# Kernel optimization log

Measured on AMD Instinct MI355X. Metric: run time of the kernel, lower is better.

Reference implementation:

```python
import jax, jax.numpy as jnp
import numpy as np

NEG_SLOPE = 0.2  # LeakyReLU slope used by GAT attention
EPS = 1e-16


def gat_conv(x, edge_index, W, a_src, a_dst, b):
    """One GATConv layer with 'mean' head aggregation.
    x: [N, Fin], edge_index: [2, E] (row 0 = src/j, row 1 = dst/i),
    W: [Fin, H*F], a_src/a_dst: [H, F], b: [F].
    Returns [N, F].
    """
    N = x.shape[0]
    H, F = a_src.shape
    h = (x @ W).reshape(N, H, F)                      # [N, H, F]
    src, dst = edge_index[0], edge_index[1]
    # per-node attention halves, gathered per edge
    as_ = jnp.einsum('nhf,hf->nh', h, a_src)          # [N, H]
    ad_ = jnp.einsum('nhf,hf->nh', h, a_dst)          # [N, H]
    e = jax.nn.leaky_relu(as_[src] + ad_[dst], NEG_SLOPE)  # [E, H]
    # segment softmax over incoming edges of each dst node
    m = jax.ops.segment_max(e, dst, num_segments=N)   # [N, H]
    ex = jnp.exp(e - m[dst])                          # [E, H]
    denom = jax.ops.segment_sum(ex, dst, num_segments=N)
    alpha = ex / (denom[dst] + EPS)                   # [E, H]
    # weighted scatter-aggregate of source features
    out = jax.ops.segment_sum(alpha[:, :, None] * h[src], dst, num_segments=N)  # [N, H, F]
    return out.mean(axis=1) + b                       # mean over heads


def setup_inputs() -> dict:
    key = jax.random.key(0)
    ks = jax.random.split(key, 10)
    N, E = 100000, 1000000
    in_dim, hid, out_dim, H = 128, 32, 16, 4
    x = jax.random.normal(ks[0], (N, in_dim), dtype=jnp.float32)
    edge_index = jax.random.randint(ks[1], (2, E), 0, N, dtype=jnp.int64)
    s1 = 1.0 / np.sqrt(in_dim)
    s2 = 1.0 / np.sqrt(hid)
    W1 = jax.random.uniform(ks[2], (in_dim, H * hid), jnp.float32, -s1, s1)
    a1_src = jax.random.uniform(ks[3], (H, hid), jnp.float32, -s2, s2)
    a1_dst = jax.random.uniform(ks[4], (H, hid), jnp.float32, -s2, s2)
    b1 = jnp.zeros((hid,), jnp.float32)
    s3 = 1.0 / np.sqrt(out_dim)
    W2 = jax.random.uniform(ks[5], (hid, H * out_dim), jnp.float32, -s2, s2)
    a2_src = jax.random.uniform(ks[6], (H, out_dim), jnp.float32, -s3, s3)
    a2_dst = jax.random.uniform(ks[7], (H, out_dim), jnp.float32, -s3, s3)
    b2 = jnp.zeros((out_dim,), jnp.float32)
    return {"x": x, "edge_index": edge_index,
            "W1": W1, "a1_src": a1_src, "a1_dst": a1_dst, "b1": b1,
            "W2": W2, "a2_src": a2_src, "a2_dst": a2_dst, "b2": b2}


def reference(x, edge_index, W1, a1_src, a1_dst, b1, W2, a2_src, a2_dst, b2):
    h = gat_conv(x, edge_index, W1, a1_src, a1_dst, b1)
    h = jax.nn.relu(h)
    # dropout is identity in eval mode
    out = gat_conv(h, edge_index, W2, a2_src, a2_dst, b2)
    return out
```

## Files before the change

### kernel.cpp

```cpp
#include <hip/hip_runtime.h>
#include <math.h>

#define NEG_SLOPE 0.2f
#define EPS_GAT 1e-16f
#define LOG2E 1.4426950408889634f
typedef unsigned int u32;
typedef unsigned short u16;
typedef __attribute__((ext_vector_type(8))) short short8;
typedef __attribute__((ext_vector_type(4))) float f32x4;

__device__ inline u16 f2bf(float x) {
    union { float f; u32 u; } v; v.f = x;
    u32 r = v.u + 0x7FFFu + ((v.u >> 16) & 1u);
    return (u16)(r >> 16);
}
__device__ inline float bf_lo(u32 u) {
    union { u32 i; float f; } v; v.i = u << 16; return v.f;
}
__device__ inline float bf_hi(u32 u) {
    union { u32 i; float f; } v; v.i = u & 0xFFFF0000u; return v.f;
}
__device__ inline float bf1(u16 s) {
    union { u32 i; float f; } v; v.i = ((u32)s) << 16; return v.f;
}
__device__ inline float fast_exp2(float x) {
#if __has_builtin(__builtin_amdgcn_exp2f)
    return __builtin_amdgcn_exp2f(x);
#else
    return exp2f(x);
#endif
}
__device__ inline float lrelu_exp2(float t) {
    return fast_exp2(fmaxf(t, NEG_SLOPE * t));
}


__global__ void degree_prep_kernel(const int* __restrict__ dst, int E,
                                   int* __restrict__ counts, int* __restrict__ rank,
                                   const float* __restrict__ W1,
                                   u16* __restrict__ w1t_hi, u16* __restrict__ w1t_lo,
                                   const float* __restrict__ W2, const float* __restrict__ a2s,
                                   const float* __restrict__ a2d, float* __restrict__ w_as,
                                   float* __restrict__ w_ad, int degBlocks) {
    int b = blockIdx.x;
    if (b < degBlocks) {
        int e = b * 256 + threadIdx.x;
        if (e < E) rank[e] = atomicAdd(&counts[dst[e]], 1);
    } else if (b < degBlocks + 64) {
        int i = (b - degBlocks) * 256 + threadIdx.x;
        int k = i >> 7, n = i & 127;
        float w = W1[i];
        u16 hi = f2bf(w);
        u16 lo = f2bf(w - bf1(hi));
        w1t_hi[n * 128 + k] = hi;
        w1t_lo[n * 128 + k] = lo;
    } else {
        int t = threadIdx.x;
        if (t < 128) {
            int h = t >> 5, k = t & 31;
            float s1 = 0.f, s2 = 0.f;
#pragma unroll
            for (int f = 0; f < 16; ++f) {
                float w = W2[k * 64 + h * 16 + f];
                s1 += w * a2s[h * 16 + f];
                s2 += w * a2d[h * 16 + f];
            }
            w_as[h * 32 + k] = s1;
            w_ad[h * 32 + k] = s2;
        }
    }
}

__global__ __launch_bounds__(1024) void scan_block_kernel(const int* __restrict__ counts, int N,
                                                          int* __restrict__ scanned, int* __restrict__ bsums) {
    __shared__ int tmp[1024];
    int i = blockIdx.x * 1024 + threadIdx.x;
    int v = (i < N) ? counts[i] : 0;
    tmp[threadIdx.x] = v;
    __syncthreads();
    for (int d = 1; d < 1024; d <<= 1) {
        int t = (threadIdx.x >= d) ? tmp[threadIdx.x - d] : 0;
        __syncthreads();
        tmp[threadIdx.x] += t;
        __syncthreads();
    }
    if (i < N) scanned[i] = tmp[threadIdx.x];
    if (threadIdx.x == 1023) bsums[blockIdx.x] = tmp[1023];
}

__global__ __launch_bounds__(256) void scan_partials_kernel(int* __restrict__ bsums, int nb) {
    __shared__ int tmp[256];
    int tid = threadIdx.x;
    int v = (tid < nb) ? bsums[tid] : 0;
    tmp[tid] = v;
    __syncthreads();
    for (int d = 1; d < 256; d <<= 1) {
        int t = (tid >= d) ? tmp[tid - d] : 0;
        __syncthreads();
        tmp[tid] += t;
        __syncthreads();
    }
    if (tid < nb) bsums[tid] = tmp[tid] - v;
}

__global__ void finalize_offsets_kernel(const int* __restrict__ scanned,
                                        const int* __restrict__ bsums_excl, int N,
                                        int* __restrict__ row_off) {
    int i = blockIdx.x * blockDim.x + threadIdx.x;
    if (i < N) {
        int incl = scanned[i] + bsums_excl[i >> 10];
        row_off[i + 1] = incl;
        if (i == 0) row_off[0] = 0;
    }
}

__global__ void fill_csr_kernel(const int* __restrict__ src, const int* __restrict__ dst, int E,
                                const int* __restrict__ row_off, const int* __restrict__ rank,
                                int* __restrict__ csr_src) {
    int e = blockIdx.x * blockDim.x + threadIdx.x;
    if (e < E) {
        int pos = row_off[dst[e]] + rank[e];
        csr_src[pos] = src[e];
    }
}


__global__ __launch_bounds__(256) void gemm1_mfma_kernel(const float* __restrict__ X,
                                                         const u16* __restrict__ w1t_hi,
                                                         const u16* __restrict__ w1t_lo,
                                                         const float* __restrict__ a_src,
                                                         const float* __restrict__ a_dst,
                                                         u16* __restrict__ Hb,
                                                         float* __restrict__ as_,
                                                         float* __restrict__ ad_, int N) {
    __shared__ u16 xsh_hi[64][40];
    __shared__ u16 xsh_lo[64][40];
    __shared__ u16 wbuf[10240];
    __shared__ float ash[128], adsh[128];
    u16* wsh_hi = wbuf;
    u16* wsh_lo = wbuf + 5120;
    int tid = threadIdx.x;
    int wave = tid >> 6, lane = tid & 63, quad = lane >> 4;
    int m0 = blockIdx.x * 64;

    if (tid < 128) { ash[tid] = a_src[tid]; adsh[tid] = a_dst[tid]; }

    f32x4 acc[4][2];
#pragma unroll
    for (int rt = 0; rt < 4; ++rt)
#pragma unroll
        for (int ct = 0; ct < 2; ++ct) acc[rt][ct] = (f32x4)(0.f);

    int xrow = tid >> 2, xkq = (tid & 3) * 8;

    for (int k0 = 0; k0 < 128; k0 += 32) {
        {
            int gr = m0 + xrow;
            float f[8];
            *(float4*)&f[0] = (gr < N) ? *(const float4*)(X + (size_t)gr * 128 + k0 + xkq)
                                       : make_float4(0.f, 0.f, 0.f, 0.f);
            *(float4*)&f[4] = (gr < N) ? *(const float4*)(X + (size_t)gr * 128 + k0 + xkq + 4)
                                       : make_float4(0.f, 0.f, 0.f, 0.f);
            u16 hi[8], lo[8];
#pragma unroll
            for (int i = 0; i < 8; ++i) {
                hi[i] = f2bf(f[i]);
                lo[i] = f2bf(f[i] - bf1(hi[i]));
            }
            *(uint4*)&xsh_hi[xrow][xkq] = *(uint4*)hi;
            *(uint4*)&xsh_lo[xrow][xkq] = *(uint4*)lo;
        }
        {
#pragma unroll
            for (int i = 0; i < 2; ++i) {
                int id = tid * 2 + i;
                int n = id >> 2, part = id & 3;
                *(uint4*)&wsh_hi[n * 40 + part * 8] =
                    ((const uint4*)(w1t_hi + n * 128 + k0))[part];
                *(uint4*)&wsh_lo[n * 40 + part * 8] =
                    ((const uint4*)(w1t_lo + n * 128 + k0))[part];
            }
        }
        __syncthreads();

        short8 bhi[2], blo[2];
#pragma unroll
        for (int ct = 0; ct < 2; ++ct) {
            int n = wave * 32 + ct * 16 + (lane & 15);
            bhi[ct] = *(const short8*)&wsh_hi[n * 40 + quad * 8];
            blo[ct] = *(const short8*)&wsh_lo[n * 40 + quad * 8];
        }
#pragma unroll
        for (int rt = 0; rt < 4; ++rt) {
            int m = rt * 16 + (lane & 15);
            short8 ahi = *(const short8*)&xsh_hi[m][quad * 8];
            short8 alo = *(const short8*)&xsh_lo[m][quad * 8];
#pragma unroll
            for (int ct = 0; ct < 2; ++ct) {
                acc[rt][ct] = __builtin_amdgcn_mfma_f32_16x16x32_bf16(ahi, bhi[ct], acc[rt][ct], 0, 0, 0);
                acc[rt][ct] = __builtin_amdgcn_mfma_f32_16x16x32_bf16(alo, bhi[ct], acc[rt][ct], 0, 0, 0);
                acc[rt][ct] = __builtin_amdgcn_mfma_f32_16x16x32_bf16(ahi, blo[ct], acc[rt][ct], 0, 0, 0);
            }
        }
        __syncthreads();
    }

    const int HS = 130;
#pragma unroll
    for (int rt = 0; rt < 4; ++rt)
#pragma unroll
        for (int ct = 0; ct < 2; ++ct) {
            int col = wave * 32 + ct * 16 + (lane & 15);
#pragma unroll
            for (int r = 0; r < 4; ++r) {
                int row = rt * 16 + quad * 4 + r;
                u16 hv = f2bf(acc[rt][ct][r]);
                int gr = m0 + row;
                if (gr < N) Hb[(size_t)gr * 128 + col] = hv;
                wbuf[row * HS + col] = hv;
            }
        }
    __syncthreads();

    {
        int row = tid >> 2, h = tid & 3;
        int gr = m0 + row;
        if (gr < N) {
            const u32* hr = (const u32*)&wbuf[row * HS + h * 32];
            float s1 = 0.f, s2 = 0.f;
#pragma unroll
            for (int q = 0; q < 16; ++q) {
                u32 u = hr[q];
                float flo = bf_lo(u), fhi = bf_hi(u);
                s1 += flo * ash[h * 32 + 2 * q] + fhi * ash[h * 32 + 2 * q + 1];
                s2 += flo * adsh[h * 32 + 2 * q] + fhi * adsh[h * 32 + 2 * q + 1];
            }
            as_[(size_t)gr * 4 + h] = s1 * LOG2E;
            ad_[(size_t)gr * 4 + h] = s2 * LOG2E;
        }
    }
}


__global__ __launch_bounds__(256) void node_agg128_kernel(const u32* __restrict__ Hb,
                                                          const float* __restrict__ as_,
                                                          const float* __restrict__ ad_,
                                                          const int* __restrict__ row_off,
                                                          const int* __restrict__ csr_src,
                                                          const float* __restrict__ bias,
                                                          const float* __restrict__ w_as,
                                                          const float* __restrict__ w_ad,
                                                          u32* __restrict__ O1,
                                                          float* __restrict__ as2,
                                                          float* __restrict__ ad2, int N) {
    int lane = threadIdx.x & 63;
    int node = __builtin_amdgcn_readfirstlane(blockIdx.x * 4 + (threadIdx.x >> 6));
    if (node >= N) return;
    int start = __builtin_amdgcn_readfirstlane(row_off[node]);
    int end   = __builtin_amdgcn_readfirstlane(row_off[node + 1]);
    int deg = end - start;
    int h = lane >> 4;
    float adh = ad_[node * 4 + h];

    int clamp = (deg > 0) ? deg - 1 : 0;
    int vidx = csr_src[start + min(lane, clamp)];
    int m = min(deg, 64);

    float2 acc = make_float2(0.f, 0.f);
    float den = 0.f;
    int j = 0;
    for (; j + 4 <= m; j += 4) {
        int s0 = __builtin_amdgcn_readlane(vidx, j);
        int s1 = __builtin_amdgcn_readlane(vidx, j + 1);
        int s2 = __builtin_amdgcn_readlane(vidx, j + 2);
        int s3 = __builtin_amdgcn_readlane(vidx, j + 3);
        float a0 = as_[s0 * 4 + h], a1 = as_[s1 * 4 + h];
        float a2 = as_[s2 * 4 + h], a3 = as_[s3 * 4 + h];
        u32 u0 = Hb[s0 * 64 + lane];
        u32 u1 = Hb[s1 * 64 + lane];
        u32 u2 = Hb[s2 * 64 + lane];
        u32 u3 = Hb[s3 * 64 + lane];
        float e0 = lrelu_exp2(a0 + adh), e1 = lrelu_exp2(a1 + adh);
        float e2 = lrelu_exp2(a2 + adh), e3 = lrelu_exp2(a3 + adh);
        acc.x = fmaf(e0, bf_lo(u0), acc.x); acc.y = fmaf(e0, bf_hi(u0), acc.y); den += e0;
        acc.x = fmaf(e1, bf_lo(u1), acc.x); acc.y = fmaf(e1, bf_hi(u1), acc.y); den += e1;
        acc.x = fmaf(e2, bf_lo(u2), acc.x); acc.y = fmaf(e2, bf_hi(u2), acc.y); den += e2;
        acc.x = fmaf(e3, bf_lo(u3), acc.x); acc.y = fmaf(e3, bf_hi(u3), acc.y); den += e3;
    }
    for (; j < m; ++j) {
        int s = __builtin_amdgcn_readlane(vidx, j);
        float e = lrelu_exp2(as_[s * 4 + h] + adh);
        u32 u = Hb[s * 64 + lane];
        acc.x = fmaf(e, bf_lo(u), acc.x); acc.y = fmaf(e, bf_hi(u), acc.y); den += e;
    }
    for (int jj = start + 64; jj < end; ++jj) {
        int s = __builtin_amdgcn_readfirstlane(csr_src[jj]);
        float e = lrelu_exp2(as_[s * 4 + h] + adh);
        u32 u = Hb[s * 64 + lane];
        acc.x = fmaf(e, bf_lo(u), acc.x); acc.y = fmaf(e, bf_hi(u), acc.y); den += e;
    }
    float inv = 1.f / (den + EPS_GAT);
    float px = acc.x * inv, py = acc.y * inv;
    px += __shfl_xor(px, 16); py += __shfl_xor(py, 16);
    px += __shfl_xor(px, 32); py += __shfl_xor(py, 32);

    int f2 = (lane & 15) * 2;
    float2 bv = *(const float2*)&bias[f2];
    float ox = fmaxf(px * 0.25f + bv.x, 0.f);
    float oy = fmaxf(py * 0.25f + bv.y, 0.f);
    if (lane < 16)
        O1[node * 16 + lane] = (u32)f2bf(ox) | ((u32)f2bf(oy) << 16);

    int h2 = lane >> 4;
    float2 wa = *(const float2*)&w_as[h2 * 32 + f2];
    float2 wd = *(const float2*)&w_ad[h2 * 32 + f2];
    float ta = ox * wa.x + oy * wa.y;
    float td = ox * wd.x + oy * wd.y;
    ta += __shfl_xor(ta, 1); td += __shfl_xor(td, 1);
    ta += __shfl_xor(ta, 2); td += __shfl_xor(td, 2);
    ta += __shfl_xor(ta, 4); td += __shfl_xor(td, 4);
    ta += __shfl_xor(ta, 8); td += __shfl_xor(td, 8);
    if ((lane & 15) == 0) {
        as2[node * 4 + h2] = ta * LOG2E;
        ad2[node * 4 + h2] = td * LOG2E;
    }
}


__global__ __launch_bounds__(256) void node_agg32_fused_kernel(const u32* __restrict__ O1,
                                                               const float* __restrict__ as_,
                                                               const float* __restrict__ ad_,
                                                               const int* __restrict__ row_off,
                                                               const int* __restrict__ csr_src,
                                                               const float* __restrict__ W2,
                                                               const float* __restrict__ b2,
                                                               float* __restrict__ Out, int N) {
    __shared__ float w2sh[2048];
    __shared__ float aggsh[4][136];
    int tid = threadIdx.x;
    {
        float4 v = ((const float4*)W2)[tid];
        *(float4*)&w2sh[tid * 4] = v;
        float4 v2 = ((const float4*)W2)[tid + 256];
        *(float4*)&w2sh[(tid + 256) * 4] = v2;
    }

    int lane = tid & 63;
    int nb = tid >> 6;
    int node = __builtin_amdgcn_readfirstlane(blockIdx.x * 4 + nb);
    bool active = node < N;
    int h = lane >> 4, f = lane & 15;
    if (active) {
        int start = __builtin_amdgcn_readfirstlane(row_off[node]);
        int end   = __builtin_amdgcn_readfirstlane(row_off[node + 1]);
        int deg = end - start;
        float adh = ad_[node * 4 + h];

        int clamp = (deg > 0) ? deg - 1 : 0;
        int vidx = csr_src[start + min(lane, clamp)];
        int m = min(deg, 64);

        float2 acc = make_float2(0.f, 0.f);
        float den = 0.f;
        int j = 0;
        for (; j + 4 <= m; j += 4) {
            int s0 = __builtin_amdgcn_readlane(vidx, j);
            int s1 = __builtin_amdgcn_readlane(vidx, j + 1);
            int s2 = __builtin_amdgcn_readlane(vidx, j + 2);
            int s3 = __builtin_amdgcn_readlane(vidx, j + 3);
            float a0 = as_[s0 * 4 + h], a1 = as_[s1 * 4 + h];
            float a2 = as_[s2 * 4 + h], a3 = as_[s3 * 4 + h];
            u32 u0 = O1[s0 * 16 + f];
            u32 u1 = O1[s1 * 16 + f];
            u32 u2 = O1[s2 * 16 + f];
            u32 u3 = O1[s3 * 16 + f];
            float e0 = lrelu_exp2(a0 + adh), e1 = lrelu_exp2(a1 + adh);
            float e2 = lrelu_exp2(a2 + adh), e3 = lrelu_exp2(a3 + adh);
            acc.x = fmaf(e0, bf_lo(u0), acc.x); acc.y = fmaf(e0, bf_hi(u0), acc.y); den += e0;
            acc.x = fmaf(e1, bf_lo(u1), acc.x); acc.y = fmaf(e1, bf_hi(u1), acc.y); den += e1;
            acc.x = fmaf(e2, bf_lo(u2), acc.x); acc.y = fmaf(e2, bf_hi(u2), acc.y); den += e2;
            acc.x = fmaf(e3, bf_lo(u3), acc.x); acc.y = fmaf(e3, bf_hi(u3), acc.y); den += e3;
        }
        for (; j < m; ++j) {
            int s = __builtin_amdgcn_readlane(vidx, j);
            float e = lrelu_exp2(as_[s * 4 + h] + adh);
            u32 u = O1[s * 16 + f];
            acc.x = fmaf(e, bf_lo(u), acc.x); acc.y = fmaf(e, bf_hi(u), acc.y); den += e;
        }
        for (int jj = start + 64; jj < end; ++jj) {
            int s = __builtin_amdgcn_readfirstlane(csr_src[jj]);
            float e = lrelu_exp2(as_[s * 4 + h] + adh);
            u32 u = O1[s * 16 + f];
            acc.x = fmaf(e, bf_lo(u), acc.x); acc.y = fmaf(e, bf_hi(u), acc.y); den += e;
        }
        float inv = 1.f / (den + EPS_GAT);
        aggsh[nb][h * 34 + f * 2]     = acc.x * inv;
        aggsh[nb][h * 34 + f * 2 + 1] = acc.y * inv;
    }
    __syncthreads();

    if (active) {
        int q = h, o = f;
        float s = 0.f;
#pragma unroll
        for (int k = 0; k < 32; ++k)
            s += aggsh[nb][q * 34 + k] * w2sh[k * 64 + q * 16 + o];
        s += __shfl_xor(s, 16);
        s += __shfl_xor(s, 32);
        if (lane < 16)
            Out[(size_t)node * 16 + o] = s * 0.25f + b2[o];
    }
}


extern "C" void kernel_launch(void* const* d_in, const int* in_sizes, int n_in,
                              void* d_out, int out_size, void* d_ws, size_t ws_size,
                              hipStream_t stream) {
    const float* x      = (const float*)d_in[0];
    const int*   eidx   = (const int*)d_in[1];
    const float* W1     = (const float*)d_in[2];
    const float* a1_src = (const float*)d_in[3];
    const float* a1_dst = (const float*)d_in[4];
    const float* b1     = (const float*)d_in[5];
    const float* W2     = (const float*)d_in[6];
    const float* a2_src = (const float*)d_in[7];
    const float* a2_dst = (const float*)d_in[8];
    const float* b2     = (const float*)d_in[9];
    float* out = (float*)d_out;

    const int N = in_sizes[0] / 128;
    const int E = in_sizes[1] / 2;
    const int* src = eidx;
    const int* dst = eidx + E;

    char* base = (char*)d_ws;
    size_t off = 0;
    auto carve = [&](size_t bytes) -> char* {
        off = (off + 255) & ~(size_t)255;
        char* p = base + off;
        off += bytes;
        return p;
    };
    int* counts   = (int*)carve((size_t)N * 4);
    int* scanned  = (int*)carve((size_t)N * 4);
    int* bsums    = (int*)carve(256 * 4);
    int* row_off  = (int*)carve((size_t)(N + 1) * 4);
    int* rank     = (int*)carve((size_t)E * 4);
    int* csr_src  = (int*)carve((size_t)E * 4);
    u16* w1t_hi   = (u16*)carve(128 * 128 * 2);
    u16* w1t_lo   = (u16*)carve(128 * 128 * 2);
    u16* h1b      = (u16*)carve((size_t)N * 128 * 2);
    u32* out1b    = (u32*)carve((size_t)N * 16 * 4);
    float* as1  = (float*)carve((size_t)N * 4 * 4);
    float* ad1  = (float*)carve((size_t)N * 4 * 4);
    float* as2  = (float*)carve((size_t)N * 4 * 4);
    float* ad2  = (float*)carve((size_t)N * 4 * 4);
    float* w_as = (float*)carve(4 * 32 * 4);
    float* w_ad = (float*)carve(4 * 32 * 4);
    (void)ws_size; (void)n_in; (void)out_size;

    hipMemsetAsync(counts, 0, (size_t)N * 4, stream);
    int degBlocks = (E + 255) / 256;
    degree_prep_kernel<<<degBlocks + 65, 256, 0, stream>>>(dst, E, counts, rank,
                                                           W1, w1t_hi, w1t_lo,
                                                           W2, a2_src, a2_dst, w_as, w_ad,
                                                           degBlocks);
    int nb = (N + 1023) / 1024;
    scan_block_kernel<<<nb, 1024, 0, stream>>>(counts, N, scanned, bsums);
    scan_partials_kernel<<<1, 256, 0, stream>>>(bsums, nb);
    finalize_offsets_kernel<<<(N + 255) / 256, 256, 0, stream>>>(scanned, bsums, N, row_off);
    fill_csr_kernel<<<(E + 255) / 256, 256, 0, stream>>>(src, dst, E, row_off, rank, csr_src);

    gemm1_mfma_kernel<<<(N + 63) / 64, 256, 0, stream>>>(x, w1t_hi, w1t_lo, a1_src, a1_dst,
                                                         h1b, as1, ad1, N);
    node_agg128_kernel<<<(N + 3) / 4, 256, 0, stream>>>((const u32*)h1b, as1, ad1,
                                                        row_off, csr_src, b1, w_as, w_ad,
                                                        out1b, as2, ad2, N);

    node_agg32_fused_kernel<<<(N + 3) / 4, 256, 0, stream>>>(out1b, as2, ad2, row_off,
                                                             csr_src, W2, b2, out, N);
}
```

Before: 298.5 us.

## Fuse CSR build kernels, overlap degree counting with GEMM, widen layer-2 gather

Result: no change. 300.9 us (+0.8%).

```diff
diff --git a/kernel.cpp b/kernel.cpp
--- a/kernel.cpp
+++ b/kernel.cpp
@@ -35,123 +35,76 @@
 }
 
 
-__global__ void degree_prep_kernel(const int* __restrict__ dst, int E,
-                                   int* __restrict__ counts, int* __restrict__ rank,
-                                   const float* __restrict__ W1,
-                                   u16* __restrict__ w1t_hi, u16* __restrict__ w1t_lo,
-                                   const float* __restrict__ W2, const float* __restrict__ a2s,
-                                   const float* __restrict__ a2d, float* __restrict__ w_as,
-                                   float* __restrict__ w_ad, int degBlocks) {
-    int b = blockIdx.x;
-    if (b < degBlocks) {
-        int e = b * 256 + threadIdx.x;
-        if (e < E) rank[e] = atomicAdd(&counts[dst[e]], 1);
-    } else if (b < degBlocks + 64) {
-        int i = (b - degBlocks) * 256 + threadIdx.x;
+__global__ void prep_kernel(const float* __restrict__ W1,
+                            u16* __restrict__ w1t_hi, u16* __restrict__ w1t_lo,
+                            const float* __restrict__ W2, const float* __restrict__ a2s,
+                            const float* __restrict__ a2d, float* __restrict__ w_as,
+                            float* __restrict__ w_ad, int* __restrict__ counts, int N,
+                            int* __restrict__ done) {
+    int g = blockIdx.x * 256 + threadIdx.x;
+    int gs = gridDim.x * 256;
+    for (int i = g; i < N; i += gs) counts[i] = 0;
+    if (g == 0) *done = 0;
+    for (int i = g; i < 16384; i += gs) {
         int k = i >> 7, n = i & 127;
         float w = W1[i];
         u16 hi = f2bf(w);
         u16 lo = f2bf(w - bf1(hi));
         w1t_hi[n * 128 + k] = hi;
         w1t_lo[n * 128 + k] = lo;
-    } else {
-        int t = threadIdx.x;
-        if (t < 128) {
-            int h = t >> 5, k = t & 31;
-            float s1 = 0.f, s2 = 0.f;
-#pragma unroll
-            for (int f = 0; f < 16; ++f) {
-                float w = W2[k * 64 + h * 16 + f];
-                s1 += w * a2s[h * 16 + f];
-                s2 += w * a2d[h * 16 + f];
-            }
-            w_as[h * 32 + k] = s1;
-            w_ad[h * 32 + k] = s2;
-        }
-    }
-}
-
-__global__ __launch_bounds__(1024) void scan_block_kernel(const int* __restrict__ counts, int N,
-                                                          int* __restrict__ scanned, int* __restrict__ bsums) {
-    __shared__ int tmp[1024];
-    int i = blockIdx.x * 1024 + threadIdx.x;
-    int v = (i < N) ? counts[i] : 0;
-    tmp[threadIdx.x] = v;
-    __syncthreads();
-    for (int d = 1; d < 1024; d <<= 1) {
-        int t = (threadIdx.x >= d) ? tmp[threadIdx.x - d] : 0;
-        __syncthreads();
-        tmp[threadIdx.x] += t;
-        __syncthreads();
-    }
-    if (i < N) scanned[i] = tmp[threadIdx.x];
-    if (threadIdx.x == 1023) bsums[blockIdx.x] = tmp[1023];
-}
-
-__global__ __launch_bounds__(256) void scan_partials_kernel(int* __restrict__ bsums, int nb) {
-    __shared__ int tmp[256];
+    }
+    if (g < 128) {
+        int h = g >> 5, k = g & 31;
+        float s1 = 0.f, s2 = 0.f;
+#pragma unroll
+        for (int f = 0; f < 16; ++f) {
+            float w = W2[k * 64 + h * 16 + f];
+            s1 += w * a2s[h * 16 + f];
+            s2 += w * a2d[h * 16 + f];
+        }
+        w_as[h * 32 + k] = s1;
+        w_ad[h * 32 + k] = s2;
+    }
+}
+
+
+__global__ __launch_bounds__(256) void gemm1_degree_kernel(const int* __restrict__ dst, int E,
+                                                           int* __restrict__ counts,
+                                                           int* __restrict__ rank,
+                                                           const float* __restrict__ X,
+                                                           const u16* __restrict__ w1t_hi,
+                                                           const u16* __restrict__ w1t_lo,
+                                                           const float* __restrict__ a_src,
+                                                           const float* __restrict__ a_dst,
+                                                           u16* __restrict__ Hb,
+                                                           float* __restrict__ as_,
+                                                           float* __restrict__ ad_,
+                                                           int N, int degBlocks) {
+    __shared__ __align__(16) u16 xsh_hi[64 * 40];
+    __shared__ __align__(16) u16 xsh_lo[64 * 40];
+    __shared__ __align__(16) u16 wbuf[10240];
+    __shared__ float ash[128], adsh[128];
+
     int tid = threadIdx.x;
-    int v = (tid < nb) ? bsums[tid] : 0;
-    tmp[tid] = v;
-    __syncthreads();
-    for (int d = 1; d < 256; d <<= 1) {
-        int t = (tid >= d) ? tmp[tid - d] : 0;
-        __syncthreads();
-        tmp[tid] += t;
-        __syncthreads();
-    }
-    if (tid < nb) bsums[tid] = tmp[tid] - v;
-}
-
-__global__ void finalize_offsets_kernel(const int* __restrict__ scanned,
-                                        const int* __restrict__ bsums_excl, int N,
-                                        int* __restrict__ row_off) {
-    int i = blockIdx.x * blockDim.x + threadIdx.x;
-    if (i < N) {
-        int incl = scanned[i] + bsums_excl[i >> 10];
-        row_off[i + 1] = incl;
-        if (i == 0) row_off[0] = 0;
-    }
-}
-
-__global__ void fill_csr_kernel(const int* __restrict__ src, const int* __restrict__ dst, int E,
-                                const int* __restrict__ row_off, const int* __restrict__ rank,
-                                int* __restrict__ csr_src) {
-    int e = blockIdx.x * blockDim.x + threadIdx.x;
-    if (e < E) {
-        int pos = row_off[dst[e]] + rank[e];
-        csr_src[pos] = src[e];
-    }
-}
-
-
-__global__ __launch_bounds__(256) void gemm1_mfma_kernel(const float* __restrict__ X,
-                                                         const u16* __restrict__ w1t_hi,
-                                                         const u16* __restrict__ w1t_lo,
-                                                         const float* __restrict__ a_src,
-                                                         const float* __restrict__ a_dst,
-                                                         u16* __restrict__ Hb,
-                                                         float* __restrict__ as_,
-                                                         float* __restrict__ ad_, int N) {
-    __shared__ u16 xsh_hi[64][40];
-    __shared__ u16 xsh_lo[64][40];
-    __shared__ u16 wbuf[10240];
-    __shared__ float ash[128], adsh[128];
+    if ((int)blockIdx.x < degBlocks) {
+        int stride = degBlocks * 256;
+        for (int e = blockIdx.x * 256 + tid; e < E; e += stride)
+            rank[e] = atomicAdd(&counts[dst[e]], 1);
+        return;
+    }
+    int m0 = (blockIdx.x - degBlocks) * 64;
+
+    if (tid < 128) { ash[tid] = a_src[tid]; adsh[tid] = a_dst[tid]; }
     u16* wsh_hi = wbuf;
     u16* wsh_lo = wbuf + 5120;
-    int tid = threadIdx.x;
     int wave = tid >> 6, lane = tid & 63, quad = lane >> 4;
-    int m0 = blockIdx.x * 64;
-
-    if (tid < 128) { ash[tid] = a_src[tid]; adsh[tid] = a_dst[tid]; }
+    int xrow = tid >> 2, xkq = (tid & 3) * 8;
 
     f32x4 acc[4][2];
 #pragma unroll
     for (int rt = 0; rt < 4; ++rt)
 #pragma unroll
         for (int ct = 0; ct < 2; ++ct) acc[rt][ct] = (f32x4)(0.f);
-
-    int xrow = tid >> 2, xkq = (tid & 3) * 8;
 
     for (int k0 = 0; k0 < 128; k0 += 32) {
         {
@@ -167,8 +120,8 @@
                 hi[i] = f2bf(f[i]);
                 lo[i] = f2bf(f[i] - bf1(hi[i]));
             }
-            *(uint4*)&xsh_hi[xrow][xkq] = *(uint4*)hi;
-            *(uint4*)&xsh_lo[xrow][xkq] = *(uint4*)lo;
+            *(uint4*)&xsh_hi[xrow * 40 + xkq] = *(uint4*)hi;
+            *(uint4*)&xsh_lo[xrow * 40 + xkq] = *(uint4*)lo;
         }
         {
 #pragma unroll
@@ -193,8 +146,8 @@
 #pragma unroll
         for (int rt = 0; rt < 4; ++rt) {
             int m = rt * 16 + (lane & 15);
-            short8 ahi = *(const short8*)&xsh_hi[m][quad * 8];
-            short8 alo = *(const short8*)&xsh_lo[m][quad * 8];
+            short8 ahi = *(const short8*)&xsh_hi[m * 40 + quad * 8];
+            short8 alo = *(const short8*)&xsh_lo[m * 40 + quad * 8];
 #pragma unroll
             for (int ct = 0; ct < 2; ++ct) {
                 acc[rt][ct] = __builtin_amdgcn_mfma_f32_16x16x32_bf16(ahi, bhi[ct], acc[rt][ct], 0, 0, 0);
@@ -238,6 +191,64 @@
             as_[(size_t)gr * 4 + h] = s1 * LOG2E;
             ad_[(size_t)gr * 4 + h] = s2 * LOG2E;
         }
+    }
+}
+
+
+__global__ __launch_bounds__(1024) void scan_kernel(const int* __restrict__ counts, int N,
+                                                    int* __restrict__ scanned,
+                                                    int* __restrict__ bsums,
+                                                    int* __restrict__ done, int nchunks) {
+    __shared__ int tmp[1024];
+    __shared__ int flag;
+    int tid = threadIdx.x;
+    int i = (blockIdx.x << 10) + tid;
+    int v = (i < N) ? counts[i] : 0;
+    tmp[tid] = v;
+    __syncthreads();
+    for (int d = 1; d < 1024; d <<= 1) {
+        int t = (tid >= d) ? tmp[tid - d] : 0;
+        __syncthreads();
+        tmp[tid] += t;
+        __syncthreads();
+    }
+    if (i < N) scanned[i] = tmp[tid];
+    if (tid == 1023) bsums[blockIdx.x] = tmp[1023];
+    __syncthreads();
+    if (tid == 0) {
+        __threadfence();
+        int prev = atomicAdd(done, 1);
+        flag = (prev == (int)gridDim.x - 1);
+    }
+    __syncthreads();
+    if (flag) {
+        __threadfence();
+        int vv = (tid < nchunks) ? bsums[tid] : 0;
+        tmp[tid] = vv;
+        __syncthreads();
+        for (int d = 1; d < 1024; d <<= 1) {
+            int t = (tid >= d) ? tmp[tid - d] : 0;
+            __syncthreads();
+            tmp[tid] += t;
+            __syncthreads();
+        }
+        if (tid < nchunks) bsums[tid] = tmp[tid] - vv;
+    }
+}
+
+
+__global__ void fill_finalize_kernel(const int* __restrict__ src, const int* __restrict__ dst,
+                                     int E, int N, const int* __restrict__ counts,
+                                     const int* __restrict__ scanned, const int* __restrict__ bsums,
+                                     const int* __restrict__ rank, int* __restrict__ row_off,
+                                     int* __restrict__ csr_src) {
+    int t = blockIdx.x * blockDim.x + threadIdx.x;
+    if (t <= N)
+        row_off[t] = (t == 0) ? 0 : scanned[t - 1] + bsums[(t - 1) >> 10];
+    if (t < E) {
+        int d = dst[t];
+        int startd = scanned[d] + bsums[d >> 10] - counts[d];
+        csr_src[startd + rank[t]] = src[t];
     }
 }
 
@@ -336,7 +347,7 @@
                                                                const float* __restrict__ b2,
                                                                float* __restrict__ Out, int N) {
     __shared__ float w2sh[2048];
-    __shared__ float aggsh[4][136];
+    __shared__ float aggsh[4][144];
     int tid = threadIdx.x;
     {
         float4 v = ((const float4*)W2)[tid];
@@ -349,62 +360,76 @@
     int nb = tid >> 6;
     int node = __builtin_amdgcn_readfirstlane(blockIdx.x * 4 + nb);
     bool active = node < N;
-    int h = lane >> 4, f = lane & 15;
+    int eg = lane >> 5;
+    int hh = (lane >> 3) & 3;
+    int fl = lane & 7;
     if (active) {
         int start = __builtin_amdgcn_readfirstlane(row_off[node]);
         int end   = __builtin_amdgcn_readfirstlane(row_off[node + 1]);
         int deg = end - start;
-        float adh = ad_[node * 4 + h];
+        float adh = ad_[node * 4 + hh];
 
         int clamp = (deg > 0) ? deg - 1 : 0;
         int vidx = csr_src[start + min(lane, clamp)];
         int m = min(deg, 64);
 
-        float2 acc = make_float2(0.f, 0.f);
+        float4 acc = make_float4(0.f, 0.f, 0.f, 0.f);
         float den = 0.f;
         int j = 0;
         for (; j + 4 <= m; j += 4) {
-            int s0 = __builtin_amdgcn_readlane(vidx, j);
-            int s1 = __builtin_amdgcn_readlane(vidx, j + 1);
-            int s2 = __builtin_amdgcn_readlane(vidx, j + 2);
-            int s3 = __builtin_amdgcn_readlane(vidx, j + 3);
-            float a0 = as_[s0 * 4 + h], a1 = as_[s1 * 4 + h];
-            float a2 = as_[s2 * 4 + h], a3 = as_[s3 * 4 + h];
-            u32 u0 = O1[s0 * 16 + f];
-            u32 u1 = O1[s1 * 16 + f];
-            u32 u2 = O1[s2 * 16 + f];
-            u32 u3 = O1[s3 * 16 + f];
-            float e0 = lrelu_exp2(a0 + adh), e1 = lrelu_exp2(a1 + adh);
-            float e2 = lrelu_exp2(a2 + adh), e3 = lrelu_exp2(a3 + adh);
-            acc.x = fmaf(e0, bf_lo(u0), acc.x); acc.y = fmaf(e0, bf_hi(u0), acc.y); den += e0;
-            acc.x = fmaf(e1, bf_lo(u1), acc.x); acc.y = fmaf(e1, bf_hi(u1), acc.y); den += e1;
-            acc.x = fmaf(e2, bf_lo(u2), acc.x); acc.y = fmaf(e2, bf_hi(u2), acc.y); den += e2;
-            acc.x = fmaf(e3, bf_lo(u3), acc.x); acc.y = fmaf(e3, bf_hi(u3), acc.y); den += e3;
-        }
-        for (; j < m; ++j) {
-            int s = __builtin_amdgcn_readlane(vidx, j);
-            float e = lrelu_exp2(as_[s * 4 + h] + adh);
-            u32 u = O1[s * 16 + f];
-            acc.x = fmaf(e, bf_lo(u), acc.x); acc.y = fmaf(e, bf_hi(u), acc.y); den += e;
-        }
-        for (int jj = start + 64; jj < end; ++jj) {
-            int s = __builtin_amdgcn_readfirstlane(csr_src[jj]);
-            float e = lrelu_exp2(as_[s * 4 + h] + adh);
-            u32 u = O1[s * 16 + f];
-            acc.x = fmaf(e, bf_lo(u), acc.x); acc.y = fmaf(e, bf_hi(u), acc.y); den += e;
-        }
+            int sA = __shfl(vidx, j + eg);
+            int sB = __shfl(vidx, j + 2 + eg);
+            uint2 uA = *(const uint2*)(O1 + sA * 16 + fl * 2);
+            uint2 uB = *(const uint2*)(O1 + sB * 16 + fl * 2);
+            float aA = as_[sA * 4 + hh];
+            float aB = as_[sB * 4 + hh];
+            float eA = lrelu_exp2(aA + adh);
+            float eB = lrelu_exp2(aB + adh);
+            den += eA + eB;
+            acc.x = fmaf(eA, bf_lo(uA.x), acc.x); acc.y = fmaf(eA, bf_hi(uA.x), acc.y);
+            acc.z = fmaf(eA, bf_lo(uA.y), acc.z); acc.w = fmaf(eA, bf_hi(uA.y), acc.w);
+            acc.x = fmaf(eB, bf_lo(uB.x), acc.x); acc.y = fmaf(eB, bf_hi(uB.x), acc.y);
+            acc.z = fmaf(eB, bf_lo(uB.y), acc.z); acc.w = fmaf(eB, bf_hi(uB.y), acc.w);
+        }
+        for (; j < m; j += 2) {
+            int jj = j + eg;
+            int s = __shfl(vidx, (jj < m) ? jj : j);
+            uint2 u = *(const uint2*)(O1 + s * 16 + fl * 2);
+            float e = lrelu_exp2(as_[s * 4 + hh] + adh);
+            if (jj >= m) e = 0.f;
+            den += e;
+            acc.x = fmaf(e, bf_lo(u.x), acc.x); acc.y = fmaf(e, bf_hi(u.x), acc.y);
+            acc.z = fmaf(e, bf_lo(u.y), acc.z); acc.w = fmaf(e, bf_hi(u.y), acc.w);
+        }
+        for (int jj2 = start + 64; jj2 < end; ++jj2) {
+            int s = __builtin_amdgcn_readfirstlane(csr_src[jj2]);
+            if (eg == 0) {
+                uint2 u = *(const uint2*)(O1 + s * 16 + fl * 2);
+                float e = lrelu_exp2(as_[s * 4 + hh] + adh);
+                den += e;
+                acc.x = fmaf(e, bf_lo(u.x), acc.x); acc.y = fmaf(e, bf_hi(u.x), acc.y);
+                acc.z = fmaf(e, bf_lo(u.y), acc.z); acc.w = fmaf(e, bf_hi(u.y), acc.w);
+            }
+        }
+        den   += __shfl_xor(den, 32);
+        acc.x += __shfl_xor(acc.x, 32);
+        acc.y += __shfl_xor(acc.y, 32);
+        acc.z += __shfl_xor(acc.z, 32);
+        acc.w += __shfl_xor(acc.w, 32);
         float inv = 1.f / (den + EPS_GAT);
-        aggsh[nb][h * 34 + f * 2]     = acc.x * inv;
-        aggsh[nb][h * 34 + f * 2 + 1] = acc.y * inv;
+        if (eg == 0) {
+            float4 o = make_float4(acc.x * inv, acc.y * inv, acc.z * inv, acc.w * inv);
+            *(float4*)&aggsh[nb][hh * 36 + fl * 4] = o;
+        }
     }
     __syncthreads();
 
     if (active) {
-        int q = h, o = f;
+        int q = lane >> 4, o = lane & 15;
         float s = 0.f;
 #pragma unroll
         for (int k = 0; k < 32; ++k)
-            s += aggsh[nb][q * 34 + k] * w2sh[k * 64 + q * 16 + o];
+            s += aggsh[nb][q * 36 + k] * w2sh[k * 64 + q * 16 + o];
         s += __shfl_xor(s, 16);
         s += __shfl_xor(s, 32);
         if (lane < 16)
@@ -443,10 +468,11 @@
     };
     int* counts   = (int*)carve((size_t)N * 4);
     int* scanned  = (int*)carve((size_t)N * 4);
-    int* bsums    = (int*)carve(256 * 4);
+    int* bsums    = (int*)carve(1024 * 4);
+    int* done     = (int*)carve(256);
     int* row_off  = (int*)carve((size_t)(N + 1) * 4);
     int* rank     = (int*)carve((size_t)E * 4);
-    int* csr_src  = (int*)carve((size_t)E * 4);
+    int* csr_src  = (int*)carve(((size_t)E + 64) * 4);
     u16* w1t_hi   = (u16*)carve(128 * 128 * 2);
     u16* w1t_lo   = (u16*)carve(128 * 128 * 2);
     u16* h1b      = (u16*)carve((size_t)N * 128 * 2);
@@ -459,20 +485,26 @@
     float* w_ad = (float*)carve(4 * 32 * 4);
     (void)ws_size; (void)n_in; (void)out_size;
 
-    hipMemsetAsync(counts, 0, (size_t)N * 4, stream);
-    int degBlocks = (E + 255) / 256;
-    degree_prep_kernel<<<degBlocks + 65, 256, 0, stream>>>(dst, E, counts, rank,
-                                                           W1, w1t_hi, w1t_lo,
-                                                           W2, a2_src, a2_dst, w_as, w_ad,
-                                                           degBlocks);
-    int nb = (N + 1023) / 1024;
-    scan_block_kernel<<<nb, 1024, 0, stream>>>(counts, N, scanned, bsums);
-    scan_partials_kernel<<<1, 256, 0, stream>>>(bsums, nb);
-    finalize_offsets_kernel<<<(N + 255) / 256, 256, 0, stream>>>(scanned, bsums, N, row_off);
-    fill_csr_kernel<<<(E + 255) / 256, 256, 0, stream>>>(src, dst, E, row_off, rank, csr_src);
-
-    gemm1_mfma_kernel<<<(N + 63) / 64, 256, 0, stream>>>(x, w1t_hi, w1t_lo, a1_src, a1_dst,
-                                                         h1b, as1, ad1, N);
+    prep_kernel<<<256, 256, 0, stream>>>(W1, w1t_hi, w1t_lo, W2, a2_src, a2_dst,
+                                         w_as, w_ad, counts, N, done);
+
+    int degBlocks = 1024;
+    int tiles = (N + 63) / 64;
+    gemm1_degree_kernel<<<degBlocks + tiles, 256, 0, stream>>>(dst, E, counts, rank,
+                                                               x, w1t_hi, w1t_lo,
+                                                               a1_src, a1_dst,
+                                                               h1b, as1, ad1, N, degBlocks);
+
+    int nchunks = (N + 1023) / 1024;
+    scan_kernel<<<nchunks, 1024, 0, stream>>>(counts, N, scanned, bsums, done, nchunks);
+
+    {
+        int total = (E > N + 1) ? E : (N + 1);
+        fill_finalize_kernel<<<(total + 255) / 256, 256, 0, stream>>>(src, dst, E, N, counts,
+                                                                      scanned, bsums, rank,
+                                                                      row_off, csr_src);
+    }
+
     node_agg128_kernel<<<(N + 3) / 4, 256, 0, stream>>>((const u32*)h1b, as1, ad1,
                                                         row_off, csr_src, b1, w_as, w_ad,
                                                         out1b, as2, ad2, N);
```
